# Kernel optimization log

Hardware: AMD Instinct MI355X
Metric: run time of the kernel (lower is better)

The kernel has to match this reference:

```python
import jax, jax.numpy as jnp
import numpy as np


def setup_inputs() -> dict:
    key = jax.random.key(0)
    k1, k2, k3, k4, k5 = jax.random.split(key, 5)
    B, S, IC, OC = 4, 2048, 4096, 4096
    n_out = int(0.05 * IC)  # 204 outlier columns
    return {
        "x": jax.random.normal(k1, (B, S, IC), dtype=jnp.float32),
        "weight": jax.random.normal(k2, (OC, IC), dtype=jnp.float32) * 0.02,
        "bias": jax.random.normal(k3, (OC,), dtype=jnp.float32) * 0.02,
        "outlier_weight": jax.random.normal(k4, (OC, n_out), dtype=jnp.float32) * 0.02,
        "outlier_columns_index": jax.random.randint(k5, (n_out,), 0, IC, dtype=jnp.int32),
    }


def reference(x, weight, bias, outlier_weight, outlier_columns_index):
    # XnorBinaryLinear.quant_weight: per-output-row mean-centering,
    # sign binarization, scaled by per-row mean absolute value.
    mean = jnp.mean(weight, axis=1, keepdims=True)            # [OC, 1]
    centered = weight - mean                                  # [OC, IC]
    scale = jnp.mean(jnp.abs(centered), axis=1, keepdims=True)  # [OC, 1]
    q = jnp.sign(centered) * scale                            # binarized weight [OC, IC]
    # scatter fp32 outlier columns back into the binarized weight
    w = q.at[:, outlier_columns_index].set(outlier_weight)    # [OC, IC]
    # F.linear(x, w, bias) = x @ w.T + bias
    out = jnp.einsum('bsi,oi->bso', x, w) + bias
    return out
```

## Files before the change

### kernel.cpp

```cpp
#include <hip/hip_runtime.h>
#include <hip/hip_bf16.h>


typedef __attribute__((ext_vector_type(4))) int i32x4;

__global__ void quant_sign_kernel(const float* __restrict__ w,
                                  const float* __restrict__ ow,
                                  const int* __restrict__ idx,
                                  signed char* __restrict__ qw,
                                  float* __restrict__ sArr,
                                  int IC, int K2, int n_out) {
    __shared__ float red[8];
    __shared__ signed char sgn[4096];
    __shared__ int cmL[4096];
    const int o = blockIdx.x;
    const int t = threadIdx.x;
    const int lane = t & 63, wid = t >> 6;

#pragma unroll
    for (int i = 0; i < 16; ++i) cmL[t + i * 256] = -1;

    const float4* row4 = (const float4*)(w + (size_t)o * IC);
    float4 v[4];
    float s = 0.f;
#pragma unroll
    for (int j = 0; j < 4; ++j) {
        v[j] = row4[t + j * 256];
        s += v[j].x + v[j].y + v[j].z + v[j].w;
    }
#pragma unroll
    for (int off = 32; off; off >>= 1) s += __shfl_down(s, off);
    if (lane == 0) red[wid] = s;
    __syncthreads();
    const float mean = (red[0] + red[1] + red[2] + red[3]) / (float)IC;

    if (t < n_out) atomicMax(&cmL[idx[t]], t);

    float a = 0.f;
#pragma unroll
    for (int j = 0; j < 4; ++j)
        a += fabsf(v[j].x - mean) + fabsf(v[j].y - mean) +
             fabsf(v[j].z - mean) + fabsf(v[j].w - mean);
#pragma unroll
    for (int off = 32; off; off >>= 1) a += __shfl_down(a, off);
    if (lane == 0) red[4 + wid] = a;
    __syncthreads();
    const float scale = (red[4] + red[5] + red[6] + red[7]) / (float)IC;
    if (t == 0) sArr[o] = scale;

    const size_t base = (size_t)o * K2;
#pragma unroll
    for (int j = 0; j < 4; ++j) {
        const int c0 = (t + j * 256) * 4;
        float ee[4] = {v[j].x, v[j].y, v[j].z, v[j].w};
        int pack = 0;
#pragma unroll
        for (int ei = 0; ei < 4; ++ei) {
            float c = ee[ei] - mean;
            int q = c > 0.f ? 8 : (c < 0.f ? -8 : 0);
            pack |= (q & 0xff) << (ei * 8);
        }
        *(int*)(qw + base + c0) = pack;
        *(int*)(sgn + c0) = pack;
    }
    __syncthreads();

    signed char q = 0;
    if (t < n_out) {
        const int c = idx[t];
        if (cmL[c] == t) {
            const float sg = (float)sgn[c] * 0.125f;
            const float wc = ow[(size_t)o * n_out + t] - scale * sg;
            float qf = rintf(8.f * wc / scale);
            qf = fminf(127.f, fmaxf(-127.f, qf));
            q = (signed char)(int)qf;
        }
    }
    qw[base + IC + t] = q;
}

__global__ void quant_x_kernel(const float4* __restrict__ x4,
                               const int* __restrict__ idx,
                               signed char* __restrict__ qx,
                               float* __restrict__ rdel,
                               int IC, int K2, int n_out) {
    __shared__ float red[4];
    __shared__ float bmax;
    __shared__ signed char rowq[4096];
    const int m = blockIdx.x;
    const int t = threadIdx.x;
    const int lane = t & 63, wid = t >> 6;

    const float4* row4 = x4 + (size_t)m * (IC / 4);
    float4 v[4];
    float mx = 0.f;
#pragma unroll
    for (int j = 0; j < 4; ++j) {
        v[j] = row4[t + j * 256];
        mx = fmaxf(mx, fmaxf(fmaxf(fabsf(v[j].x), fabsf(v[j].y)),
                             fmaxf(fabsf(v[j].z), fabsf(v[j].w))));
    }
#pragma unroll
    for (int off = 32; off; off >>= 1) mx = fmaxf(mx, __shfl_down(mx, off));
    if (lane == 0) red[wid] = mx;
    __syncthreads();
    if (t == 0) {
        float m0 = fmaxf(fmaxf(red[0], red[1]), fmaxf(red[2], red[3]));
        bmax = m0;
        rdel[m] = m0 / 127.f;
    }
    __syncthreads();
    const float inv = 127.f / bmax;

    const size_t base = (size_t)m * K2;
#pragma unroll
    for (int j = 0; j < 4; ++j) {
        const int c0 = (t + j * 256) * 4;
        float ee[4] = {v[j].x, v[j].y, v[j].z, v[j].w};
        int pack = 0;
#pragma unroll
        for (int ei = 0; ei < 4; ++ei) {
            int q = (int)rintf(ee[ei] * inv);
            pack |= (q & 0xff) << (ei * 8);
        }
        *(int*)(qx + base + c0) = pack;
        *(int*)(rowq + c0) = pack;
    }
    __syncthreads();

    signed char g = 0;
    if (t < n_out) g = rowq[idx[t]];
    qx[base + IC + t] = g;
}

#define GLDS(src, dst) __builtin_amdgcn_global_load_lds( \
    (const __attribute__((address_space(1))) void*)(src), \
    (__attribute__((address_space(3))) void*)(dst), 16, 0, 0)

#define STAGE64(MAT, bufS, knB) do {                                          \
    const signed char* gsrc_ = (MAT) ? Bblk : Ablk;                           \
    _Pragma("unroll")                                                         \
    for (int rr_ = 0; rr_ < 2; ++rr_) {                                       \
      GLDS(gsrc_ + (size_t)(rr_ * 128 + stg_row) * K2 + (knB) + stg_col,      \
           &ldsb[(bufS) * 32768 + (MAT) * 16384 + (rr_ * 128 + wid * 16) * 64]); \
    } } while (0)

#define RDA(AF, FH, B_) do {                                                  \
    const signed char* pa_ = &ldsb[(B_) * 32768];                             \
    _Pragma("unroll")                                                         \
    for (int j_ = 0; j_ < 4; ++j_)                                            \
      AF[j_] = *(const i32x4*)&pa_[(wr * 128 + ((FH) * 4 + j_) * 16 + l15) * 64 + slB]; \
  } while (0)

#define RDB(BF, B_) do {                                                      \
    const signed char* pb_ = &ldsb[(B_) * 32768 + 16384];                     \
    _Pragma("unroll")                                                         \
    for (int j_ = 0; j_ < 4; ++j_)                                            \
      BF[j_] = *(const i32x4*)&pb_[(wc * 64 + j_ * 16 + l15) * 64 + slB];     \
  } while (0)

#define MM16(AF, FH) do {                                                     \
    _Pragma("unroll")                                                         \
    for (int mi_ = 0; mi_ < 4; ++mi_)                                         \
      _Pragma("unroll")                                                       \
      for (int ni_ = 0; ni_ < 4; ++ni_)                                       \
        acc[(FH) * 4 + mi_][ni_] = __builtin_amdgcn_mfma_i32_16x16x64_i8(     \
            AF[mi_], bfr[ni_], acc[(FH) * 4 + mi_][ni_], 0, 0, 0);            \
  } while (0)

#define KT64(bufR, bufS, knB) do {                                            \
    RDB(bfr, bufR);                                                           \
    RDA(afr0, 0, bufR);                                                       \
    RDA(afr1, 1, bufR);                                                       \
    STAGE64(0, bufS, knB);                                                    \
    STAGE64(1, bufS, knB);                                                    \
    __builtin_amdgcn_s_setprio(1);                                            \
    MM16(afr0, 0);                                                            \
    MM16(afr1, 1);                                                            \
    __builtin_amdgcn_s_setprio(0);                                            \
    asm volatile("s_waitcnt vmcnt(8)" ::: "memory");                          \
    __builtin_amdgcn_s_barrier();                                             \
  } while (0)

__global__ __launch_bounds__(512, 2) void gemm_i8_kernel(
    const signed char* __restrict__ Aq,
    const signed char* __restrict__ Bq,
    const float* __restrict__ bias,
    const float* __restrict__ sArr,
    const float* __restrict__ rdel,
    float* __restrict__ C,
    int M, int N, int K2, int NBN) {
    extern __shared__ signed char ldsb[];

    const int t = threadIdx.x;
    const int wid = t >> 6, lane = t & 63;
    const int l15 = lane & 15;
    const int slB = (((lane >> 4) ^ ((lane >> 1) & 3)) & 3) * 16;
    const int wr = wid >> 2;
    const int wc = wid & 3;
    const int stg_row = wid * 16 + (lane >> 2);
    const int stg_col = (((lane & 3) ^ ((lane >> 3) & 3)) & 3) * 16;

    const int nwg = gridDim.x;
    const int bid = blockIdx.x;
    const int q = nwg >> 3, r = nwg & 7;
    const int xcd = bid & 7, off = bid >> 3;
    const int swz = (xcd < r ? xcd * (q + 1) : r * (q + 1) + (xcd - r) * q) + off;
    const int bm = swz / NBN, bn = swz % NBN;

    const signed char* Ablk = Aq + (size_t)(bm * 256) * K2;
    const signed char* Bblk = Bq + (size_t)(bn * 256) * K2;

    i32x4 acc[8][4] = {};
    i32x4 afr0[4], afr1[4], bfr[4];

    STAGE64(0, 0, 0);    STAGE64(1, 0, 0);
    STAGE64(0, 1, 64);   STAGE64(1, 1, 64);
    STAGE64(0, 2, 128);  STAGE64(1, 2, 128);
    asm volatile("s_waitcnt vmcnt(8)" ::: "memory");
    __builtin_amdgcn_s_barrier();

    for (int it = 0; it < 17; ++it) {
        const int tt = it * 4;
        const int k3 = (tt + 3) * 64;
        const int k4 = (tt + 4 < 68) ? (tt + 4) * 64 : 0;
        const int k5 = (tt + 5 < 68) ? (tt + 5) * 64 : 0;
        const int k6 = (tt + 6 < 68) ? (tt + 6) * 64 : 0;
        KT64(0, 3, k3);
        KT64(1, 0, k4);
        KT64(2, 1, k5);
        KT64(3, 2, k6);
    }

    float sv[4], bv[4];
#pragma unroll
    for (int ni = 0; ni < 4; ++ni) {
        const int col = bn * 256 + wc * 64 + ni * 16 + l15;
        sv[ni] = sArr[col] * 0.125f;
        bv[ni] = bias[col];
    }

    const int crow0 = bm * 256 + wr * 128;
    const int ccol = bn * 256 + wc * 64 + l15;
#pragma unroll
    for (int mi = 0; mi < 8; ++mi) {
#pragma unroll
        for (int rr = 0; rr < 4; ++rr) {
            const int row = crow0 + mi * 16 + (lane >> 4) * 4 + rr;
            const float rd = rdel[row];
            float* Crow = C + (size_t)row * N;
#pragma unroll
            for (int ni = 0; ni < 4; ++ni)
                Crow[ccol + ni * 16] =
                    (float)acc[mi][ni][rr] * (sv[ni] * rd) + bv[ni];
        }
    }
}

extern "C" void kernel_launch(void* const* d_in, const int* in_sizes, int n_in,
                              void* d_out, int out_size, void* d_ws, size_t ws_size,
                              hipStream_t stream) {
    const float* x      = (const float*)d_in[0];
    const float* weight = (const float*)d_in[1];
    const float* bias   = (const float*)d_in[2];
    const float* ow     = (const float*)d_in[3];
    const int*   idx    = (const int*)d_in[4];

    const int OC    = in_sizes[2];
    const int n_out = in_sizes[4];
    const int IC    = in_sizes[1] / OC;
    const int M     = in_sizes[0] / IC;
    const int K2    = IC + 256;
    float* out = (float*)d_out;

    char* ws = (char*)d_ws;
    signed char* qx = (signed char*)ws;
    signed char* qw = (signed char*)(ws + (size_t)M * K2);
    float* sArr = (float*)(ws + (size_t)M * K2 + (size_t)OC * K2);
    float* rdel = sArr + OC;

    quant_sign_kernel<<<OC, 256, 0, stream>>>(weight, ow, idx, qw, sArr,
                                              IC, K2, n_out);
    quant_x_kernel<<<M, 256, 0, stream>>>((const float4*)x, idx, qx, rdel,
                                          IC, K2, n_out);

    hipFuncSetAttribute((const void*)gemm_i8_kernel,
                        hipFuncAttributeMaxDynamicSharedMemorySize, 131072);
    const int NBM = M / 256, NBN = OC / 256;
    gemm_i8_kernel<<<dim3(NBM * NBN), dim3(512), 131072, stream>>>(
        qx, qw, bias, sArr, rdel, out, M, OC, K2, NBN);
}
```

Baseline: 181.1 us.

## Restructure int8 GEMM main loop to 128-wide K tiles with double buffering

```diff
diff --git a/kernel.cpp b/kernel.cpp
--- a/kernel.cpp
+++ b/kernel.cpp
@@ -137,26 +137,27 @@
     (const __attribute__((address_space(1))) void*)(src), \
     (__attribute__((address_space(3))) void*)(dst), 16, 0, 0)
 
-#define STAGE64(MAT, bufS, knB) do {                                          \
+#define STAGE128(MAT, bufS, knB) do {                                         \
     const signed char* gsrc_ = (MAT) ? Bblk : Ablk;                           \
     _Pragma("unroll")                                                         \
-    for (int rr_ = 0; rr_ < 2; ++rr_) {                                       \
-      GLDS(gsrc_ + (size_t)(rr_ * 128 + stg_row) * K2 + (knB) + stg_col,      \
-           &ldsb[(bufS) * 32768 + (MAT) * 16384 + (rr_ * 128 + wid * 16) * 64]); \
+    for (int p_ = 0; p_ < 4; ++p_) {                                          \
+      GLDS(gsrc_ + (size_t)(p_ * 64 + stg_row2) * K2 + (knB) + stg_col2,      \
+           &ldsb[(bufS) * 65536 + (MAT) * 32768 +                             \
+                 (p_ * 64 + stg_row2) * 128 + stg_dst2]);                     \
     } } while (0)
 
-#define RDA(AF, FH, B_) do {                                                  \
-    const signed char* pa_ = &ldsb[(B_) * 32768];                             \
+#define RDA(AF, FH, SL, B_) do {                                              \
+    const signed char* pa_ = &ldsb[(B_) * 65536];                             \
     _Pragma("unroll")                                                         \
     for (int j_ = 0; j_ < 4; ++j_)                                            \
-      AF[j_] = *(const i32x4*)&pa_[(wr * 128 + ((FH) * 4 + j_) * 16 + l15) * 64 + slB]; \
-  } while (0)
-
-#define RDB(BF, B_) do {                                                      \
-    const signed char* pb_ = &ldsb[(B_) * 32768 + 16384];                     \
+      AF[j_] = *(const i32x4*)&pa_[(wr * 128 + ((FH) * 4 + j_) * 16 + l15) * 128 + (SL)]; \
+  } while (0)
+
+#define RDB(BF, SL, B_) do {                                                  \
+    const signed char* pb_ = &ldsb[(B_) * 65536 + 32768];                     \
     _Pragma("unroll")                                                         \
     for (int j_ = 0; j_ < 4; ++j_)                                            \
-      BF[j_] = *(const i32x4*)&pb_[(wc * 64 + j_ * 16 + l15) * 64 + slB];     \
+      BF[j_] = *(const i32x4*)&pb_[(wc * 64 + j_ * 16 + l15) * 128 + (SL)];   \
   } while (0)
 
 #define MM16(AF, FH) do {                                                     \
@@ -168,18 +169,25 @@
             AF[mi_], bfr[ni_], acc[(FH) * 4 + mi_][ni_], 0, 0, 0);            \
   } while (0)
 
-#define KT64(bufR, bufS, knB) do {                                            \
-    RDB(bfr, bufR);                                                           \
-    RDA(afr0, 0, bufR);                                                       \
-    RDA(afr1, 1, bufR);                                                       \
-    STAGE64(0, bufS, knB);                                                    \
-    STAGE64(1, bufS, knB);                                                    \
+#define KT128(bufR, bufS, knB) do {                                           \
+    STAGE128(0, bufS, knB);                                                   \
+    STAGE128(1, bufS, knB);                                                   \
     __builtin_amdgcn_s_setprio(1);                                            \
     MM16(afr0, 0);                                                            \
     MM16(afr1, 1);                                                            \
     __builtin_amdgcn_s_setprio(0);                                            \
-    asm volatile("s_waitcnt vmcnt(8)" ::: "memory");                          \
+    RDB(bfr, slK1, bufR);                                                     \
+    RDA(afr0, 0, slK1, bufR);                                                 \
+    RDA(afr1, 1, slK1, bufR);                                                 \
+    __builtin_amdgcn_s_setprio(1);                                            \
+    MM16(afr0, 0);                                                            \
+    MM16(afr1, 1);                                                            \
+    __builtin_amdgcn_s_setprio(0);                                            \
+    asm volatile("s_waitcnt vmcnt(0)" ::: "memory");                          \
     __builtin_amdgcn_s_barrier();                                             \
+    RDB(bfr, slK0, bufS);                                                     \
+    RDA(afr0, 0, slK0, bufS);                                                 \
+    RDA(afr1, 1, slK0, bufS);                                                 \
   } while (0)
 
 __global__ __launch_bounds__(512, 2) void gemm_i8_kernel(
@@ -195,11 +203,13 @@
     const int t = threadIdx.x;
     const int wid = t >> 6, lane = t & 63;
     const int l15 = lane & 15;
-    const int slB = (((lane >> 4) ^ ((lane >> 1) & 3)) & 3) * 16;
+    const int slK0 = (((lane >> 4) ^ (lane & 7)) & 7) * 16;
+    const int slK1 = slK0 ^ 64;
     const int wr = wid >> 2;
     const int wc = wid & 3;
-    const int stg_row = wid * 16 + (lane >> 2);
-    const int stg_col = (((lane & 3) ^ ((lane >> 3) & 3)) & 3) * 16;
+    const int stg_row2 = t >> 3;
+    const int stg_col2 = (((t & 7) ^ ((t >> 3) & 7)) & 7) * 16;
+    const int stg_dst2 = (t & 7) * 16;
 
     const int nwg = gridDim.x;
     const int bid = blockIdx.x;
@@ -214,22 +224,19 @@
     i32x4 acc[8][4] = {};
     i32x4 afr0[4], afr1[4], bfr[4];
 
-    STAGE64(0, 0, 0);    STAGE64(1, 0, 0);
-    STAGE64(0, 1, 64);   STAGE64(1, 1, 64);
-    STAGE64(0, 2, 128);  STAGE64(1, 2, 128);
-    asm volatile("s_waitcnt vmcnt(8)" ::: "memory");
+    STAGE128(0, 0, 0);
+    STAGE128(1, 0, 0);
+    asm volatile("s_waitcnt vmcnt(0)" ::: "memory");
     __builtin_amdgcn_s_barrier();
+    RDB(bfr, slK0, 0);
+    RDA(afr0, 0, slK0, 0);
+    RDA(afr1, 1, slK0, 0);
 
     for (int it = 0; it < 17; ++it) {
-        const int tt = it * 4;
-        const int k3 = (tt + 3) * 64;
-        const int k4 = (tt + 4 < 68) ? (tt + 4) * 64 : 0;
-        const int k5 = (tt + 5 < 68) ? (tt + 5) * 64 : 0;
-        const int k6 = (tt + 6 < 68) ? (tt + 6) * 64 : 0;
-        KT64(0, 3, k3);
-        KT64(1, 0, k4);
-        KT64(2, 1, k5);
-        KT64(3, 2, k6);
+        const int k1 = (2 * it + 1) * 128;
+        const int k2 = (2 * it + 2 < 34) ? (2 * it + 2) * 128 : 0;
+        KT128(0, 1, k1);
+        KT128(1, 0, k2);
     }
 
     float sv[4], bv[4];
```

New measurement: 181.3 us. Within noise of the previous version (+0.1%).
